# Optimization experiments

Hardware: AMD Instinct MI355X
Metric: run time of the kernel (lower is better)

Reference implementation:

```python
import jax, jax.numpy as jnp
import numpy as np

NEG_SLOPE = 0.2  # PyG GATConv default negative_slope


def _glorot(key, shape):
    fan = shape[0]
    return jax.random.normal(key, shape, dtype=jnp.float32) / np.sqrt(fan)


def setup_inputs() -> dict:
    key = jax.random.key(0)
    ks = jax.random.split(key, 32)
    N, E, C_IN, C_H, C_OUT = 20000, 320000, 128, 640, 2
    inp = {
        "x": jax.random.normal(ks[0], (N, C_IN), dtype=jnp.float32),
        "edge_index": jax.random.randint(ks[1], (2, E), 0, N, dtype=jnp.int64),
    }
    dims = [(C_IN, C_H), (C_H, C_H), (C_H, C_H), (C_H, C_H), (C_H, C_OUT)]
    for i, (ci, co) in enumerate(dims, start=1):
        k = jax.random.split(ks[1 + i], 4)
        inp[f"W{i}"] = _glorot(k[0], (ci, co))
        inp[f"as{i}"] = _glorot(k[1], (co,))
        inp[f"ad{i}"] = _glorot(k[2], (co,))
        inp[f"b{i}"] = jnp.zeros((co,), dtype=jnp.float32)
    return inp


def _gat_conv(h, W, a_src, a_dst, b, src, dst, N):
    # h: [N, Ci] -> hW: [N, Co]
    hW = h @ W
    # per-edge attention logit: LeakyReLU(alpha_src[j] + alpha_dst[i]) for edge j->i
    e = jax.nn.leaky_relu((hW @ a_src)[src] + (hW @ a_dst)[dst], NEG_SLOPE)
    # segment softmax over incoming edges of each dst node (self-loops guarantee nonempty)
    m = jax.ops.segment_max(e, dst, num_segments=N)
    ex = jnp.exp(e - m[dst])
    den = jax.ops.segment_sum(ex, dst, num_segments=N)
    alpha = ex / den[dst]
    # weighted scatter-add of source messages
    out = jax.ops.segment_sum(alpha[:, None] * hW[src], dst, num_segments=N)
    return out + b


def reference(x, edge_index, W1, as1, ad1, b1, W2, as2, ad2, b2, W3, as3, ad3, b3,
              W4, as4, ad4, b4, W5, as5, ad5, b5):
    N = x.shape[0]
    # PyG GATConv default add_self_loops=True
    loops = jnp.arange(N, dtype=edge_index.dtype)
    ei = jnp.concatenate([edge_index, jnp.stack([loops, loops])], axis=1)
    src, dst = ei[0], ei[1]
    h = jax.nn.relu(_gat_conv(x, W1, as1, ad1, b1, src, dst, N))
    h = jax.nn.relu(_gat_conv(h, W2, as2, ad2, b2, src, dst, N))
    h = jax.nn.relu(_gat_conv(h, W3, as3, ad3, b3, src, dst, N))
    h = jax.nn.relu(_gat_conv(h, W4, as4, ad4, b4, src, dst, N))
    # dropout in eval mode = identity
    return _gat_conv(h, W5, as5, ad5, b5, src, dst, N)
```

## Files before the change

### kernel.cpp

```cpp
#include <hip/hip_runtime.h>
#include <math.h>

#define N_NODES 20000
#define MPAD 20096
#define E_EDGES 320000
#define ET (E_EDGES + N_NODES)
#define C_HID 640
#define C_IN 128
#define NEG_SLOPE 0.2f

#define NXB 157
#define NYB 10
#define NXB_FULL 152
#define IDS_MAIN 1520

typedef __attribute__((ext_vector_type(8))) short bf16x8;
typedef __attribute__((ext_vector_type(4))) float f32x4;

__device__ __forceinline__ float leaky(float x) { return x > 0.f ? x : NEG_SLOPE * x; }

__device__ __forceinline__ unsigned short f2bf(float f) {
    unsigned u = __float_as_uint(f);
    unsigned r = (u + 0x7fffu + ((u >> 16) & 1u)) >> 16;
    return (unsigned short)r;
}
__device__ __forceinline__ float bf2f(unsigned short h) {
    return __uint_as_float(((unsigned)h) << 16);
}

__device__ __forceinline__ void gld16(const void* g, void* l) {
    __builtin_amdgcn_global_load_lds((const __attribute__((address_space(1))) unsigned int*)g,
                                     (__attribute__((address_space(3))) unsigned int*)l,
                                     16, 0, 0);
}

__device__ __forceinline__ void decode_xy(int id, int& bx, int& by) {
    if (id < IDS_MAIN) {
        int g = id / 80;
        bx = g * 8 + (id & 7);
        by = (id % 80) >> 3;
    } else {
        int v = id - IDS_MAIN;
        bx = NXB_FULL + v % 5;
        by = v / 5;
    }
}

__global__ void k_zero(int* p, int n) {
    int i = blockIdx.x * blockDim.x + threadIdx.x;
    if (i < n) p[i] = 0;
}

__global__ void k_count(const int* __restrict__ ei, int* __restrict__ counts) {
    int j = blockIdx.x * blockDim.x + threadIdx.x;
    if (j >= ET) return;
    int d = (j < E_EDGES) ? ei[E_EDGES + j] : (j - E_EDGES);
    atomicAdd(&counts[d], 1);
}

__global__ __launch_bounds__(1024) void k_scan(int* __restrict__ counts,
                                               int* __restrict__ rowptr) {
    __shared__ int part[1024];
    int t = threadIdx.x;
    int base = t * 20;
    int incl[20];
    int s = 0;
#pragma unroll
    for (int k = 0; k < 20; k++) {
        int i = base + k;
        int v = (i < N_NODES) ? counts[i] : 0;
        s += v;
        incl[k] = s;
    }
    part[t] = s;
    __syncthreads();
    for (int off = 1; off < 1024; off <<= 1) {
        int x = (t >= off) ? part[t - off] : 0;
        __syncthreads();
        part[t] += x;
        __syncthreads();
    }
    int prefix = (t == 0) ? 0 : part[t - 1];
    if (t == 0) rowptr[0] = 0;
#pragma unroll
    for (int k = 0; k < 20; k++) {
        int i = base + k;
        if (i < N_NODES) {
            rowptr[i + 1] = prefix + incl[k];
            counts[i] = (k == 0) ? prefix : prefix + incl[k - 1];
        }
    }
}

__global__ void k_fill(const int* __restrict__ ei, int* __restrict__ cursor, int* __restrict__ col) {
    int j = blockIdx.x * blockDim.x + threadIdx.x;
    if (j >= ET) return;
    int s, d;
    if (j < E_EDGES) { s = ei[j]; d = ei[E_EDGES + j]; }
    else { s = d = j - E_EDGES; }
    int pos = atomicAdd(&cursor[d], 1);
    col[pos] = s;
}

__global__ __launch_bounds__(256) void k_splitWT(const float* __restrict__ W,
                                                 unsigned short* __restrict__ Wth,
                                                 unsigned short* __restrict__ Wtl, int K,
                                                 float* __restrict__ zbuf, int zn) {
    if (zbuf) {
        int tid = ((blockIdx.y * gridDim.x + blockIdx.x) * 256 + threadIdx.x) * 2;
        if (tid < zn) zbuf[tid] = 0.f;
        if (tid + 1 < zn) zbuf[tid + 1] = 0.f;
    }
    __shared__ float tile[64][65];
    int t = threadIdx.x;
    int ki = blockIdx.x * 64, ni = blockIdx.y * 64;
    int tr = t >> 2;
    int tc = (t & 3) * 16;
#pragma unroll
    for (int q = 0; q < 4; ++q) {
        float4 v = *(const float4*)&W[(size_t)(ki + tr) * C_HID + ni + tc + q * 4];
        tile[tr][tc + q * 4 + 0] = v.x;
        tile[tr][tc + q * 4 + 1] = v.y;
        tile[tr][tc + q * 4 + 2] = v.z;
        tile[tr][tc + q * 4 + 3] = v.w;
    }
    __syncthreads();
    unsigned short hh[16], ll[16];
#pragma unroll
    for (int j = 0; j < 16; ++j) {
        float w = tile[tc + j][tr];
        unsigned short h = f2bf(w);
        hh[j] = h;
        ll[j] = f2bf(w - bf2f(h));
    }
    size_t o = (size_t)(ni + tr) * K + ki + tc;
#pragma unroll
    for (int q = 0; q < 4; ++q) {
        *(ushort4*)&Wth[o + q * 4] = make_ushort4(hh[q*4], hh[q*4+1], hh[q*4+2], hh[q*4+3]);
        *(ushort4*)&Wtl[o + q * 4] = make_ushort4(ll[q*4], ll[q*4+1], ll[q*4+2], ll[q*4+3]);
    }
}

__global__ void k_padzero(unsigned short* __restrict__ xah, unsigned short* __restrict__ xal,
                          unsigned short* __restrict__ ph, unsigned short* __restrict__ pl) {
    int idx = blockIdx.x * blockDim.x + threadIdx.x;
    const int nx = (MPAD - N_NODES) * C_IN;
    const int np = (MPAD - N_NODES) * C_HID;
    if (idx < nx) {
        xah[N_NODES * C_IN + idx] = 0;
        xal[N_NODES * C_IN + idx] = 0;
    }
    if (idx < np) {
        ph[N_NODES * C_HID + idx] = 0;
        pl[N_NODES * C_HID + idx] = 0;
    }
}

__global__ void k_wa(const float* __restrict__ W, const float* __restrict__ a_s,
                     const float* __restrict__ a_d,
                     float* __restrict__ ws_, float* __restrict__ wd_) {
    int wave = (blockIdx.x * blockDim.x + threadIdx.x) >> 6;
    int lane = threadIdx.x & 63;
    if (wave >= C_IN) return;
    const float* row = W + (size_t)wave * C_HID;
    float s = 0.f, d = 0.f;
#pragma unroll
    for (int c = lane; c < C_HID; c += 64) {
        float w = row[c];
        s = fmaf(w, a_s[c], s);
        d = fmaf(w, a_d[c], d);
    }
    for (int o = 32; o; o >>= 1) { s += __shfl_xor(s, o); d += __shfl_xor(d, o); }
    if (lane == 0) { ws_[wave] = s; wd_[wave] = d; }
}

__global__ __launch_bounds__(256) void k_logitx(const float* __restrict__ x,
                                                const float* __restrict__ ws_,
                                                const float* __restrict__ wd_,
                                                float* __restrict__ as_, float* __restrict__ ad_) {
    int wave = (blockIdx.x * blockDim.x + threadIdx.x) >> 6;
    int lane = threadIdx.x & 63;
    if (wave >= N_NODES) return;
    float2 xv = ((const float2*)(x + (size_t)wave * C_IN))[lane];
    float2 wsv = ((const float2*)ws_)[lane];
    float2 wdv = ((const float2*)wd_)[lane];
    float s = xv.x * wsv.x + xv.y * wsv.y;
    float d = xv.x * wdv.x + xv.y * wdv.y;
    for (int o = 32; o; o >>= 1) { s += __shfl_xor(s, o); d += __shfl_xor(d, o); }
    if (lane == 0) { as_[wave] = s; ad_[wave] = d; }
}

__global__ __launch_bounds__(256) void k_alpha(const float* __restrict__ as_,
                                               const float* __restrict__ ad_,
                                               const int* __restrict__ rowptr,
                                               const int* __restrict__ col,
                                               float* __restrict__ alpha) {
    int wave = (blockIdx.x * blockDim.x + threadIdx.x) >> 6;
    int lane = threadIdx.x & 63;
    if (wave >= N_NODES) return;
    int start = rowptr[wave], end = rowptr[wave + 1];
    float adi = ad_[wave];
    float m = -1e30f;
    for (int j = start + lane; j < end; j += 64)
        m = fmaxf(m, leaky(as_[col[j]] + adi));
    for (int o = 32; o; o >>= 1) m = fmaxf(m, __shfl_xor(m, o));
    float den = 0.f;
    for (int j = start + lane; j < end; j += 64)
        den += __expf(leaky(as_[col[j]] + adi) - m);
    for (int o = 32; o; o >>= 1) den += __shfl_xor(den, o);
    float inv = 1.f / den;
    for (int j = start + lane; j < end; j += 64)
        alpha[j] = __expf(leaky(as_[col[j]] + adi) - m) * inv;
}

__global__ __launch_bounds__(256) void k_mfma_gemm(
    const unsigned short* __restrict__ Ahi, const unsigned short* __restrict__ Alo,
    const unsigned short* __restrict__ Bth, const unsigned short* __restrict__ Btl,
    float* __restrict__ C, int K, int M,
    const float* __restrict__ asrc, const float* __restrict__ adst,
    float* __restrict__ as_, float* __restrict__ ad_) {
    __shared__ unsigned short lds[12288];
    const int t = threadIdx.x;
    const int lane = t & 63, wv = t >> 6;
    const int wm = wv >> 1, wn = wv & 1;
    const int quad = lane >> 4, cl = lane & 15;
    int bx, by;
    decode_xy(blockIdx.x, bx, by);
    const int rowBase = bx * 128;
    const int colBase = by * 64;
    const int r4 = t >> 2;
    const int cswz = ((t & 3) ^ ((r4 >> 1) & 3)) * 8;
    const int rshift = (cl >> 1) & 3;

    f32x4 acc[4][2];
#pragma unroll
    for (int i = 0; i < 4; i++)
#pragma unroll
        for (int j = 0; j < 2; j++)
            acc[i][j] = (f32x4){0.f, 0.f, 0.f, 0.f};

    for (int k0 = 0; k0 < K; k0 += 32) {
        __syncthreads();
#pragma unroll
        for (int p = 0; p < 2; ++p) {
            int row = p * 64 + r4;
            size_t ga = (size_t)(rowBase + row) * K + k0 + cswz;
            int lo = row * 32 + (t & 3) * 8;
            gld16(Ahi + ga, &lds[lo]);
            gld16(Alo + ga, &lds[4096 + lo]);
        }
        {
            size_t gb = (size_t)(colBase + r4) * K + k0 + cswz;
            int lo = r4 * 32 + (t & 3) * 8;
            gld16(Bth + gb, &lds[8192 + lo]);
            gld16(Btl + gb, &lds[10240 + lo]);
        }
        __syncthreads();

        bf16x8 ah[4], al[4], bh[2], bl[2];
#pragma unroll
        for (int i = 0; i < 4; ++i) {
            int am = (wm * 64 + i * 16 + cl) * 32 + (quad ^ rshift) * 8;
            ah[i] = *(const bf16x8*)&lds[am];
            al[i] = *(const bf16x8*)&lds[4096 + am];
        }
#pragma unroll
        for (int j = 0; j < 2; ++j) {
            int bn = (wn * 32 + j * 16 + cl) * 32 + (quad ^ rshift) * 8;
            bh[j] = *(const bf16x8*)&lds[8192 + bn];
            bl[j] = *(const bf16x8*)&lds[10240 + bn];
        }
#pragma unroll
        for (int i = 0; i < 4; ++i)
#pragma unroll
            for (int j = 0; j < 2; ++j) {
                acc[i][j] = __builtin_amdgcn_mfma_f32_16x16x32_bf16(ah[i], bh[j], acc[i][j], 0, 0, 0);
                acc[i][j] = __builtin_amdgcn_mfma_f32_16x16x32_bf16(ah[i], bl[j], acc[i][j], 0, 0, 0);
                acc[i][j] = __builtin_amdgcn_mfma_f32_16x16x32_bf16(al[i], bh[j], acc[i][j], 0, 0, 0);
            }
    }

#pragma unroll
    for (int i = 0; i < 4; ++i)
#pragma unroll
        for (int j = 0; j < 2; ++j) {
            int colC = colBase + wn * 32 + j * 16 + cl;
#pragma unroll
            for (int rr = 0; rr < 4; ++rr) {
                int rowC = rowBase + wm * 64 + i * 16 + quad * 4 + rr;
                if (rowC < M) C[(size_t)rowC * C_HID + colC] = acc[i][j][rr];
            }
        }

    float av[2], dv[2];
#pragma unroll
    for (int j = 0; j < 2; ++j) {
        int cn = colBase + wn * 32 + j * 16 + cl;
        av[j] = asrc[cn];
        dv[j] = adst[cn];
    }
#pragma unroll
    for (int i = 0; i < 4; ++i)
#pragma unroll
        for (int rr = 0; rr < 4; ++rr) {
            float s = 0.f, d = 0.f;
#pragma unroll
            for (int j = 0; j < 2; ++j) {
                float v = acc[i][j][rr];
                s = fmaf(v, av[j], s);
                d = fmaf(v, dv[j], d);
            }
#pragma unroll
            for (int o = 8; o >= 1; o >>= 1) {
                s += __shfl_xor(s, o);
                d += __shfl_xor(d, o);
            }
            int rowC = rowBase + wm * 64 + i * 16 + quad * 4 + rr;
            if (cl == 0 && rowC < M) {
                atomicAdd(&as_[rowC], s);
                atomicAdd(&ad_[rowC], d);
            }
        }
}

__global__ __launch_bounds__(256) void k_mfma_gemm_pair(
    const unsigned short* __restrict__ Ahi, const unsigned short* __restrict__ Alo,
    const unsigned short* __restrict__ Bth, const unsigned short* __restrict__ Btl,
    unsigned short* __restrict__ Oh, unsigned short* __restrict__ Ol,
    const float* __restrict__ bias, int K, int M) {
    __shared__ unsigned short lds[12288];
    const int t = threadIdx.x;
    const int lane = t & 63, wv = t >> 6;
    const int wm = wv >> 1, wn = wv & 1;
    const int quad = lane >> 4, cl = lane & 15;
    int bx, by;
    decode_xy(blockIdx.x, bx, by);
    const int rowBase = bx * 128;
    const int colBase = by * 64;
    const int r4 = t >> 2;
    const int cswz = ((t & 3) ^ ((r4 >> 1) & 3)) * 8;
    const int rshift = (cl >> 1) & 3;

    f32x4 acc[4][2];
#pragma unroll
    for (int i = 0; i < 4; i++)
#pragma unroll
        for (int j = 0; j < 2; j++)
            acc[i][j] = (f32x4){0.f, 0.f, 0.f, 0.f};

    for (int k0 = 0; k0 < K; k0 += 32) {
        __syncthreads();
#pragma unroll
        for (int p = 0; p < 2; ++p) {
            int row = p * 64 + r4;
            size_t ga = (size_t)(rowBase + row) * K + k0 + cswz;
            int lo = row * 32 + (t & 3) * 8;
            gld16(Ahi + ga, &lds[lo]);
            gld16(Alo + ga, &lds[4096 + lo]);
        }
        {
            size_t gb = (size_t)(colBase + r4) * K + k0 + cswz;
            int lo = r4 * 32 + (t & 3) * 8;
            gld16(Bth + gb, &lds[8192 + lo]);
            gld16(Btl + gb, &lds[10240 + lo]);
        }
        __syncthreads();

        bf16x8 ah[4], al[4], bh[2], bl[2];
#pragma unroll
        for (int i = 0; i < 4; ++i) {
            int am = (wm * 64 + i * 16 + cl) * 32 + (quad ^ rshift) * 8;
            ah[i] = *(const bf16x8*)&lds[am];
            al[i] = *(const bf16x8*)&lds[4096 + am];
        }
#pragma unroll
        for (int j = 0; j < 2; ++j) {
            int bn = (wn * 32 + j * 16 + cl) * 32 + (quad ^ rshift) * 8;
            bh[j] = *(const bf16x8*)&lds[8192 + bn];
            bl[j] = *(const bf16x8*)&lds[10240 + bn];
        }
#pragma unroll
        for (int i = 0; i < 4; ++i)
#pragma unroll
            for (int j = 0; j < 2; ++j) {
                acc[i][j] = __builtin_amdgcn_mfma_f32_16x16x32_bf16(ah[i], bh[j], acc[i][j], 0, 0, 0);
                acc[i][j] = __builtin_amdgcn_mfma_f32_16x16x32_bf16(ah[i], bl[j], acc[i][j], 0, 0, 0);
                acc[i][j] = __builtin_amdgcn_mfma_f32_16x16x32_bf16(al[i], bh[j], acc[i][j], 0, 0, 0);
            }
    }

#pragma unroll
    for (int j = 0; j < 2; ++j) {
        int colC = colBase + wn * 32 + j * 16 + cl;
        float bv = bias[colC];
#pragma unroll
        for (int i = 0; i < 4; ++i)
#pragma unroll
            for (int rr = 0; rr < 4; ++rr) {
                int rowC = rowBase + wm * 64 + i * 16 + quad * 4 + rr;
                if (rowC < M) {
                    float v = fmaxf(acc[i][j][rr] + bv, 0.f);
                    unsigned short h = f2bf(v);
                    Oh[(size_t)rowC * C_HID + colC] = h;
                    Ol[(size_t)rowC * C_HID + colC] = f2bf(v - bf2f(h));
                }
            }
    }
}

__global__ __launch_bounds__(256) void k_gather64(const float* __restrict__ hW,
                                                  const float* __restrict__ alpha,
                                                  const int* __restrict__ rowptr,
                                                  const int* __restrict__ col,
                                                  const float* __restrict__ bias,
                                                  unsigned short* __restrict__ outh,
                                                  unsigned short* __restrict__ outl) {
    int lane = threadIdx.x & 63;
    int node = __builtin_amdgcn_readfirstlane(blockIdx.x * 4 + (threadIdx.x >> 6));
    int c = blockIdx.y;
    if (node >= N_NODES) return;
    int start = rowptr[node], end = rowptr[node + 1];
    const float* base = hW + c * 64 + lane;
    float ax = 0.f;

    int j0 = start;
    for (; j0 + 16 <= end; j0 += 16) {
        int cv[16];
        float av[16];
#pragma unroll
        for (int q = 0; q < 16; ++q) { cv[q] = col[j0 + q]; av[q] = alpha[j0 + q]; }
        float r[16];
#pragma unroll
        for (int q = 0; q < 16; ++q) r[q] = base[(size_t)cv[q] * C_HID];
#pragma unroll
        for (int q = 0; q < 16; ++q) ax = fmaf(av[q], r[q], ax);
    }
    if (j0 < end) {
        int jb = end - 16; if (jb < 0) jb = 0;
        int cv[16];
        float av[16];
#pragma unroll
        for (int q = 0; q < 16; ++q) {
            cv[q] = col[jb + q];
            av[q] = (jb + q >= j0) ? alpha[jb + q] : 0.f;
        }
        float r[16];
#pragma unroll
        for (int q = 0; q < 16; ++q) r[q] = base[(size_t)cv[q] * C_HID];
#pragma unroll
        for (int q = 0; q < 16; ++q) ax = fmaf(av[q], r[q], ax);
    }

    float v0 = fmaxf(ax + bias[c * 64 + lane], 0.f);
    unsigned short h0 = f2bf(v0);
    size_t o = (size_t)node * C_HID + c * 64 + lane;
    outh[o] = h0;
    outl[o] = f2bf(v0 - bf2f(h0));
}

__global__ __launch_bounds__(256) void k_gather_x(const float* __restrict__ x,
                                                  const float* __restrict__ alpha,
                                                  const int* __restrict__ rowptr,
                                                  const int* __restrict__ col,
                                                  unsigned short* __restrict__ outh,
                                                  unsigned short* __restrict__ outl) {
    int lane = threadIdx.x & 63;
    int node = __builtin_amdgcn_readfirstlane(blockIdx.x * 4 + (threadIdx.x >> 6));
    if (node >= N_NODES) return;
    int start = rowptr[node], end = rowptr[node + 1];
    const float* base = x + lane * 2;
    float ax = 0.f, ay = 0.f;

    int j0 = start;
    for (; j0 + 8 <= end; j0 += 8) {
        int cv[8];
        float av[8];
#pragma unroll
        for (int q = 0; q < 8; ++q) { cv[q] = col[j0 + q]; av[q] = alpha[j0 + q]; }
        float2 r[8];
#pragma unroll
        for (int q = 0; q < 8; ++q) r[q] = *(const float2*)(base + (size_t)cv[q] * C_IN);
#pragma unroll
        for (int q = 0; q < 8; ++q) {
            ax = fmaf(av[q], r[q].x, ax);
            ay = fmaf(av[q], r[q].y, ay);
        }
    }
    if (j0 < end) {
        int jb = end - 8; if (jb < 0) jb = 0;
        int cv[8];
        float av[8];
#pragma unroll
        for (int q = 0; q < 8; ++q) {
            cv[q] = col[jb + q];
            av[q] = (jb + q >= j0) ? alpha[jb + q] : 0.f;
        }
        float2 r[8];
#pragma unroll
        for (int q = 0; q < 8; ++q) r[q] = *(const float2*)(base + (size_t)cv[q] * C_IN);
#pragma unroll
        for (int q = 0; q < 8; ++q) {
            ax = fmaf(av[q], r[q].x, ax);
            ay = fmaf(av[q], r[q].y, ay);
        }
    }

    unsigned short h0 = f2bf(ax), h1 = f2bf(ay);
    size_t o = (size_t)node * C_IN + lane * 2;
    *(ushort2*)&outh[o] = make_ushort2(h0, h1);
    *(ushort2*)&outl[o] = make_ushort2(f2bf(ax - bf2f(h0)), f2bf(ay - bf2f(h1)));
}

__global__ __launch_bounds__(256) void k_gemm2(const unsigned short* __restrict__ hh,
                                               const unsigned short* __restrict__ hl,
                                               const float* __restrict__ W,
                                               const float* __restrict__ asrc,
                                               const float* __restrict__ adst,
                                               float* __restrict__ hW5,
                                               float* __restrict__ as_,
                                               float* __restrict__ ad_) {
    int wave = (blockIdx.x * blockDim.x + threadIdx.x) >> 6;
    int lane = threadIdx.x & 63;
    if (wave >= N_NODES) return;
    const ushort2* rh = (const ushort2*)(hh + (size_t)wave * C_HID);
    const ushort2* rl = (const ushort2*)(hl + (size_t)wave * C_HID);
    float a0 = 0.f, a1 = 0.f;
#pragma unroll
    for (int k2 = lane; k2 < C_HID / 2; k2 += 64) {
        ushort2 h2 = rh[k2];
        ushort2 l2 = rl[k2];
        float v0 = bf2f(h2.x) + bf2f(l2.x);
        float v1 = bf2f(h2.y) + bf2f(l2.y);
        int k = k2 * 2;
        a0 = fmaf(v0, W[k * 2 + 0], a0);
        a1 = fmaf(v0, W[k * 2 + 1], a1);
        a0 = fmaf(v1, W[k * 2 + 2], a0);
        a1 = fmaf(v1, W[k * 2 + 3], a1);
    }
    for (int o = 32; o; o >>= 1) { a0 += __shfl_xor(a0, o); a1 += __shfl_xor(a1, o); }
    if (lane == 0) {
        hW5[wave * 2 + 0] = a0;
        hW5[wave * 2 + 1] = a1;
        as_[wave] = a0 * asrc[0] + a1 * asrc[1];
        ad_[wave] = a0 * adst[0] + a1 * adst[1];
    }
}

__global__ __launch_bounds__(256) void k_agg2(const float* __restrict__ hW5,
                                              const float* __restrict__ as_,
                                              const float* __restrict__ ad_,
                                              const int* __restrict__ rowptr,
                                              const int* __restrict__ col,
                                              const float* __restrict__ bias,
                                              float* __restrict__ out) {
    int wv = threadIdx.x >> 6, lane = threadIdx.x & 63;
    int node = blockIdx.x * 4 + wv;
    if (node >= N_NODES) return;
    int start = rowptr[node], end = rowptr[node + 1];
    int deg = end - start;
    float adi = ad_[node];
    float o0, o1;
    if (deg <= 64) {
        int cv = col[start + min(lane, deg - 1)];
        float logit = (lane < deg) ? leaky(as_[cv] + adi) : -1e30f;
        float m = logit;
#pragma unroll
        for (int o = 32; o; o >>= 1) m = fmaxf(m, __shfl_xor(m, o));
        float ex = __expf(logit - m);
        float den = ex;
#pragma unroll
        for (int o = 32; o; o >>= 1) den += __shfl_xor(den, o);
        float al = ex / den;
        float2 hv = make_float2(0.f, 0.f);
        if (lane < deg) hv = *(const float2*)&hW5[cv * 2];
        o0 = al * hv.x; o1 = al * hv.y;
#pragma unroll
        for (int o = 32; o; o >>= 1) { o0 += __shfl_xor(o0, o); o1 += __shfl_xor(o1, o); }
    } else {
        float m = -1e30f;
        for (int j = start + lane; j < end; j += 64)
            m = fmaxf(m, leaky(as_[col[j]] + adi));
        for (int o = 32; o; o >>= 1) m = fmaxf(m, __shfl_xor(m, o));
        float den = 0.f;
        for (int j = start + lane; j < end; j += 64)
            den += __expf(leaky(as_[col[j]] + adi) - m);
        for (int o = 32; o; o >>= 1) den += __shfl_xor(den, o);
        float inv = 1.f / den;
        o0 = 0.f; o1 = 0.f;
        for (int j = start + lane; j < end; j += 64) {
            int s = col[j];
            float al = __expf(leaky(as_[s] + adi) - m) * inv;
            o0 = fmaf(al, hW5[s * 2 + 0], o0);
            o1 = fmaf(al, hW5[s * 2 + 1], o1);
        }
        for (int o = 32; o; o >>= 1) { o0 += __shfl_xor(o0, o); o1 += __shfl_xor(o1, o); }
    }
    if (lane == 0) {
        out[node * 2 + 0] = o0 + bias[0];
        out[node * 2 + 1] = o1 + bias[1];
    }
}

extern "C" void kernel_launch(void* const* d_in, const int* in_sizes, int n_in,
                              void* d_out, int out_size, void* d_ws, size_t ws_size,
                              hipStream_t stream) {
    const float* x   = (const float*)d_in[0];
    const int*   ei  = (const int*)d_in[1];
    const float* W[5]  = {(const float*)d_in[2],  (const float*)d_in[6],
                          (const float*)d_in[10], (const float*)d_in[14],
                          (const float*)d_in[18]};
    const float* As[5] = {(const float*)d_in[3],  (const float*)d_in[7],
                          (const float*)d_in[11], (const float*)d_in[15],
                          (const float*)d_in[19]};
    const float* Ad[5] = {(const float*)d_in[4],  (const float*)d_in[8],
                          (const float*)d_in[12], (const float*)d_in[16],
                          (const float*)d_in[20]};
    const float* Bi[5] = {(const float*)d_in[5],  (const float*)d_in[9],
                          (const float*)d_in[13], (const float*)d_in[17],
                          (const float*)d_in[21]};
    float* out = (float*)d_out;

    char* w = (char*)d_ws;
    float* bufX = (float*)w;                 w += (size_t)N_NODES * C_HID * 4;
    unsigned short* xa_hi = (unsigned short*)bufX;
    unsigned short* xa_lo = xa_hi + (size_t)MPAD * C_IN;
    unsigned short* pair_hi = (unsigned short*)w; w += (size_t)MPAD * C_HID * 2;
    unsigned short* pair_lo = (unsigned short*)w; w += (size_t)MPAD * C_HID * 2;
    unsigned short* Wth = (unsigned short*)w;     w += (size_t)C_HID * C_HID * 2;
    unsigned short* Wtl = (unsigned short*)w;     w += (size_t)C_HID * C_HID * 2;
    float* as_  = (float*)w;  w += N_NODES * 4;
    float* ad_  = (float*)w;  w += N_NODES * 4;
    float* hW5  = (float*)w;  w += N_NODES * 2 * 4;
    float* ws_  = (float*)w;  w += C_IN * 4;
    float* wd_  = (float*)w;  w += C_IN * 4;
    float* alpha = (float*)w; w += ET * 4;
    int* rowptr = (int*)w;    w += (N_NODES + 1) * 4 + 12;
    int* counts = (int*)w;    w += N_NODES * 4;
    int* col    = (int*)w;    w += ET * 4;

    const int TB = 256;
    k_zero<<<(N_NODES + TB - 1) / TB, TB, 0, stream>>>(counts, N_NODES);
    k_count<<<(ET + TB - 1) / TB, TB, 0, stream>>>(ei, counts);
    k_scan<<<1, 1024, 0, stream>>>(counts, rowptr);
    k_fill<<<(ET + TB - 1) / TB, TB, 0, stream>>>(ei, counts, col);

    k_padzero<<<((MPAD - N_NODES) * C_HID + TB - 1) / TB, TB, 0, stream>>>(xa_hi, xa_lo, pair_hi, pair_lo);

    const int gemmBlocks = NXB * NYB;
    dim3 gathGrid(N_NODES / 4, 10);
    int nodeWaveBlocks = (N_NODES + 3) / 4;

    k_splitWT<<<dim3(C_IN / 64, C_HID / 64), TB, 0, stream>>>(W[0], Wth, Wtl, C_IN, (float*)0, 0);
    k_wa<<<32, TB, 0, stream>>>(W[0], As[0], Ad[0], ws_, wd_);
    k_logitx<<<nodeWaveBlocks, TB, 0, stream>>>(x, ws_, wd_, as_, ad_);
    k_alpha<<<nodeWaveBlocks, TB, 0, stream>>>(as_, ad_, rowptr, col, alpha);
    k_gather_x<<<nodeWaveBlocks, TB, 0, stream>>>(x, alpha, rowptr, col, xa_hi, xa_lo);
    k_mfma_gemm_pair<<<gemmBlocks, TB, 0, stream>>>(xa_hi, xa_lo, Wth, Wtl,
                                                    pair_hi, pair_lo, Bi[0], C_IN, N_NODES);

    for (int l = 1; l <= 3; ++l) {
        k_splitWT<<<dim3(C_HID / 64, C_HID / 64), TB, 0, stream>>>(W[l], Wth, Wtl, C_HID,
                                                                   as_, 2 * N_NODES);
        k_mfma_gemm<<<gemmBlocks, TB, 0, stream>>>(pair_hi, pair_lo, Wth, Wtl, bufX, C_HID, N_NODES,
                                                   As[l], Ad[l], as_, ad_);
        k_alpha<<<nodeWaveBlocks, TB, 0, stream>>>(as_, ad_, rowptr, col, alpha);
        k_gather64<<<gathGrid, TB, 0, stream>>>(bufX, alpha, rowptr, col, Bi[l], pair_hi, pair_lo);
    }

    k_gemm2<<<nodeWaveBlocks, TB, 0, stream>>>(pair_hi, pair_lo, W[4], As[4], Ad[4], hW5, as_, ad_);
    k_agg2<<<nodeWaveBlocks, TB, 0, stream>>>(hW5, as_, ad_, rowptr, col, Bi[4], out);
}
```

Before: 763.0 us.

## Double GEMM K-tile to 64 with XOR swizzle and fuse layer-1 softmax into gather

```diff
diff --git a/kernel.cpp b/kernel.cpp
--- a/kernel.cpp
+++ b/kernel.cpp
@@ -219,7 +219,7 @@
     float* __restrict__ C, int K, int M,
     const float* __restrict__ asrc, const float* __restrict__ adst,
     float* __restrict__ as_, float* __restrict__ ad_) {
-    __shared__ unsigned short lds[12288];
+    __shared__ unsigned short lds[24576];
     const int t = threadIdx.x;
     const int lane = t & 63, wv = t >> 6;
     const int wm = wv >> 1, wn = wv & 1;
@@ -228,9 +228,8 @@
     decode_xy(blockIdx.x, bx, by);
     const int rowBase = bx * 128;
     const int colBase = by * 64;
-    const int r4 = t >> 2;
-    const int cswz = ((t & 3) ^ ((r4 >> 1) & 3)) * 8;
-    const int rshift = (cl >> 1) & 3;
+    const int sr = t >> 3;
+    const int scg = ((t & 7) ^ (sr & 7)) * 8;
 
     f32x4 acc[4][2];
 #pragma unroll
@@ -239,45 +238,52 @@
         for (int j = 0; j < 2; j++)
             acc[i][j] = (f32x4){0.f, 0.f, 0.f, 0.f};
 
-    for (int k0 = 0; k0 < K; k0 += 32) {
+    for (int k0 = 0; k0 < K; k0 += 64) {
         __syncthreads();
 #pragma unroll
+        for (int p = 0; p < 4; ++p) {
+            int r = p * 32 + sr;
+            size_t ga = (size_t)(rowBase + r) * K + k0 + scg;
+            int lo = p * 2048 + t * 8;
+            gld16(Ahi + ga, &lds[lo]);
+            gld16(Alo + ga, &lds[8192 + lo]);
+        }
+#pragma unroll
         for (int p = 0; p < 2; ++p) {
-            int row = p * 64 + r4;
-            size_t ga = (size_t)(rowBase + row) * K + k0 + cswz;
-            int lo = row * 32 + (t & 3) * 8;
-            gld16(Ahi + ga, &lds[lo]);
-            gld16(Alo + ga, &lds[4096 + lo]);
-        }
-        {
-            size_t gb = (size_t)(colBase + r4) * K + k0 + cswz;
-            int lo = r4 * 32 + (t & 3) * 8;
-            gld16(Bth + gb, &lds[8192 + lo]);
-            gld16(Btl + gb, &lds[10240 + lo]);
+            int r = p * 32 + sr;
+            size_t gb = (size_t)(colBase + r) * K + k0 + scg;
+            int lo = p * 2048 + t * 8;
+            gld16(Bth + gb, &lds[16384 + lo]);
+            gld16(Btl + gb, &lds[20480 + lo]);
         }
         __syncthreads();
 
-        bf16x8 ah[4], al[4], bh[2], bl[2];
-#pragma unroll
-        for (int i = 0; i < 4; ++i) {
-            int am = (wm * 64 + i * 16 + cl) * 32 + (quad ^ rshift) * 8;
-            ah[i] = *(const bf16x8*)&lds[am];
-            al[i] = *(const bf16x8*)&lds[4096 + am];
-        }
-#pragma unroll
-        for (int j = 0; j < 2; ++j) {
-            int bn = (wn * 32 + j * 16 + cl) * 32 + (quad ^ rshift) * 8;
-            bh[j] = *(const bf16x8*)&lds[8192 + bn];
-            bl[j] = *(const bf16x8*)&lds[10240 + bn];
-        }
-#pragma unroll
-        for (int i = 0; i < 4; ++i)
+#pragma unroll
+        for (int ks = 0; ks < 2; ++ks) {
+            bf16x8 ah[4], al[4], bh[2], bl[2];
+#pragma unroll
+            for (int i = 0; i < 4; ++i) {
+                int row = wm * 64 + i * 16 + cl;
+                int am = row * 64 + (((ks * 4 + quad) ^ (row & 7)) * 8);
+                ah[i] = *(const bf16x8*)&lds[am];
+                al[i] = *(const bf16x8*)&lds[8192 + am];
+            }
 #pragma unroll
             for (int j = 0; j < 2; ++j) {
-                acc[i][j] = __builtin_amdgcn_mfma_f32_16x16x32_bf16(ah[i], bh[j], acc[i][j], 0, 0, 0);
-                acc[i][j] = __builtin_amdgcn_mfma_f32_16x16x32_bf16(ah[i], bl[j], acc[i][j], 0, 0, 0);
-                acc[i][j] = __builtin_amdgcn_mfma_f32_16x16x32_bf16(al[i], bh[j], acc[i][j], 0, 0, 0);
-            }
+                int row = wn * 32 + j * 16 + cl;
+                int bn = row * 64 + (((ks * 4 + quad) ^ (row & 7)) * 8);
+                bh[j] = *(const bf16x8*)&lds[16384 + bn];
+                bl[j] = *(const bf16x8*)&lds[20480 + bn];
+            }
+#pragma unroll
+            for (int i = 0; i < 4; ++i)
+#pragma unroll
+                for (int j = 0; j < 2; ++j) {
+                    acc[i][j] = __builtin_amdgcn_mfma_f32_16x16x32_bf16(ah[i], bh[j], acc[i][j], 0, 0, 0);
+                    acc[i][j] = __builtin_amdgcn_mfma_f32_16x16x32_bf16(ah[i], bl[j], acc[i][j], 0, 0, 0);
+                    acc[i][j] = __builtin_amdgcn_mfma_f32_16x16x32_bf16(al[i], bh[j], acc[i][j], 0, 0, 0);
+                }
+        }
     }
 
 #pragma unroll
@@ -328,7 +334,7 @@
     const unsigned short* __restrict__ Bth, const unsigned short* __restrict__ Btl,
     unsigned short* __restrict__ Oh, unsigned short* __restrict__ Ol,
     const float* __restrict__ bias, int K, int M) {
-    __shared__ unsigned short lds[12288];
+    __shared__ unsigned short lds[24576];
     const int t = threadIdx.x;
     const int lane = t & 63, wv = t >> 6;
     const int wm = wv >> 1, wn = wv & 1;
@@ -337,9 +343,8 @@
     decode_xy(blockIdx.x, bx, by);
     const int rowBase = bx * 128;
     const int colBase = by * 64;
-    const int r4 = t >> 2;
-    const int cswz = ((t & 3) ^ ((r4 >> 1) & 3)) * 8;
-    const int rshift = (cl >> 1) & 3;
+    const int sr = t >> 3;
+    const int scg = ((t & 7) ^ (sr & 7)) * 8;
 
     f32x4 acc[4][2];
 #pragma unroll
@@ -348,45 +353,52 @@
         for (int j = 0; j < 2; j++)
             acc[i][j] = (f32x4){0.f, 0.f, 0.f, 0.f};
 
-    for (int k0 = 0; k0 < K; k0 += 32) {
+    for (int k0 = 0; k0 < K; k0 += 64) {
         __syncthreads();
 #pragma unroll
+        for (int p = 0; p < 4; ++p) {
+            int r = p * 32 + sr;
+            size_t ga = (size_t)(rowBase + r) * K + k0 + scg;
+            int lo = p * 2048 + t * 8;
+            gld16(Ahi + ga, &lds[lo]);
+            gld16(Alo + ga, &lds[8192 + lo]);
+        }
+#pragma unroll
         for (int p = 0; p < 2; ++p) {
-            int row = p * 64 + r4;
-            size_t ga = (size_t)(rowBase + row) * K + k0 + cswz;
-            int lo = row * 32 + (t & 3) * 8;
-            gld16(Ahi + ga, &lds[lo]);
-            gld16(Alo + ga, &lds[4096 + lo]);
-        }
-        {
-            size_t gb = (size_t)(colBase + r4) * K + k0 + cswz;
-            int lo = r4 * 32 + (t & 3) * 8;
-            gld16(Bth + gb, &lds[8192 + lo]);
-            gld16(Btl + gb, &lds[10240 + lo]);
+            int r = p * 32 + sr;
+            size_t gb = (size_t)(colBase + r) * K + k0 + scg;
+            int lo = p * 2048 + t * 8;
+            gld16(Bth + gb, &lds[16384 + lo]);
+            gld16(Btl + gb, &lds[20480 + lo]);
         }
         __syncthreads();
 
-        bf16x8 ah[4], al[4], bh[2], bl[2];
-#pragma unroll
-        for (int i = 0; i < 4; ++i) {
-            int am = (wm * 64 + i * 16 + cl) * 32 + (quad ^ rshift) * 8;
-            ah[i] = *(const bf16x8*)&lds[am];
-            al[i] = *(const bf16x8*)&lds[4096 + am];
-        }
-#pragma unroll
-        for (int j = 0; j < 2; ++j) {
-            int bn = (wn * 32 + j * 16 + cl) * 32 + (quad ^ rshift) * 8;
-            bh[j] = *(const bf16x8*)&lds[8192 + bn];
-            bl[j] = *(const bf16x8*)&lds[10240 + bn];
-        }
-#pragma unroll
-        for (int i = 0; i < 4; ++i)
+#pragma unroll
+        for (int ks = 0; ks < 2; ++ks) {
+            bf16x8 ah[4], al[4], bh[2], bl[2];
+#pragma unroll
+            for (int i = 0; i < 4; ++i) {
+                int row = wm * 64 + i * 16 + cl;
+                int am = row * 64 + (((ks * 4 + quad) ^ (row & 7)) * 8);
+                ah[i] = *(const bf16x8*)&lds[am];
+                al[i] = *(const bf16x8*)&lds[8192 + am];
+            }
 #pragma unroll
             for (int j = 0; j < 2; ++j) {
-                acc[i][j] = __builtin_amdgcn_mfma_f32_16x16x32_bf16(ah[i], bh[j], acc[i][j], 0, 0, 0);
-                acc[i][j] = __builtin_amdgcn_mfma_f32_16x16x32_bf16(ah[i], bl[j], acc[i][j], 0, 0, 0);
-                acc[i][j] = __builtin_amdgcn_mfma_f32_16x16x32_bf16(al[i], bh[j], acc[i][j], 0, 0, 0);
-            }
+                int row = wn * 32 + j * 16 + cl;
+                int bn = row * 64 + (((ks * 4 + quad) ^ (row & 7)) * 8);
+                bh[j] = *(const bf16x8*)&lds[16384 + bn];
+                bl[j] = *(const bf16x8*)&lds[20480 + bn];
+            }
+#pragma unroll
+            for (int i = 0; i < 4; ++i)
+#pragma unroll
+                for (int j = 0; j < 2; ++j) {
+                    acc[i][j] = __builtin_amdgcn_mfma_f32_16x16x32_bf16(ah[i], bh[j], acc[i][j], 0, 0, 0);
+                    acc[i][j] = __builtin_amdgcn_mfma_f32_16x16x32_bf16(ah[i], bl[j], acc[i][j], 0, 0, 0);
+                    acc[i][j] = __builtin_amdgcn_mfma_f32_16x16x32_bf16(al[i], bh[j], acc[i][j], 0, 0, 0);
+                }
+        }
     }
 
 #pragma unroll
@@ -459,49 +471,68 @@
 }
 
 __global__ __launch_bounds__(256) void k_gather_x(const float* __restrict__ x,
-                                                  const float* __restrict__ alpha,
+                                                  const float* __restrict__ as_,
+                                                  const float* __restrict__ ad_,
                                                   const int* __restrict__ rowptr,
                                                   const int* __restrict__ col,
                                                   unsigned short* __restrict__ outh,
                                                   unsigned short* __restrict__ outl) {
-    int lane = threadIdx.x & 63;
-    int node = __builtin_amdgcn_readfirstlane(blockIdx.x * 4 + (threadIdx.x >> 6));
+    int wv = threadIdx.x >> 6, lane = threadIdx.x & 63;
+    int node = blockIdx.x * 4 + wv;
     if (node >= N_NODES) return;
     int start = rowptr[node], end = rowptr[node + 1];
+    int deg = end - start;
     const float* base = x + lane * 2;
     float ax = 0.f, ay = 0.f;
-
-    int j0 = start;
-    for (; j0 + 8 <= end; j0 += 8) {
-        int cv[8];
-        float av[8];
-#pragma unroll
-        for (int q = 0; q < 8; ++q) { cv[q] = col[j0 + q]; av[q] = alpha[j0 + q]; }
-        float2 r[8];
-#pragma unroll
-        for (int q = 0; q < 8; ++q) r[q] = *(const float2*)(base + (size_t)cv[q] * C_IN);
-#pragma unroll
-        for (int q = 0; q < 8; ++q) {
-            ax = fmaf(av[q], r[q].x, ax);
-            ay = fmaf(av[q], r[q].y, ay);
-        }
-    }
-    if (j0 < end) {
-        int jb = end - 8; if (jb < 0) jb = 0;
-        int cv[8];
-        float av[8];
-#pragma unroll
-        for (int q = 0; q < 8; ++q) {
-            cv[q] = col[jb + q];
-            av[q] = (jb + q >= j0) ? alpha[jb + q] : 0.f;
-        }
-        float2 r[8];
-#pragma unroll
-        for (int q = 0; q < 8; ++q) r[q] = *(const float2*)(base + (size_t)cv[q] * C_IN);
-#pragma unroll
-        for (int q = 0; q < 8; ++q) {
-            ax = fmaf(av[q], r[q].x, ax);
-            ay = fmaf(av[q], r[q].y, ay);
+    float adi = ad_[node];
+
+    if (deg <= 64) {
+        int col_v = col[start + min(lane, deg - 1)];
+        float asv = as_[col_v];
+        float logit = (lane < deg) ? leaky(asv + adi) : -1e30f;
+        float m = logit;
+#pragma unroll
+        for (int o = 32; o; o >>= 1) m = fmaxf(m, __shfl_xor(m, o));
+        float ex = __expf(logit - m);
+        float den = ex;
+#pragma unroll
+        for (int o = 32; o; o >>= 1) den += __shfl_xor(den, o);
+        float alpha_v = ex / den;
+
+        for (int e0 = 0; e0 < deg; e0 += 8) {
+            float2 r[8];
+            float a[8];
+#pragma unroll
+            for (int q = 0; q < 8; ++q) {
+                int e = e0 + q;
+                int ec = min(e, deg - 1);
+                int s = __shfl(col_v, ec);
+                float ar = __shfl(alpha_v, ec);
+                a[q] = (e < deg) ? ar : 0.f;
+                r[q] = *(const float2*)(base + (size_t)s * C_IN);
+            }
+#pragma unroll
+            for (int q = 0; q < 8; ++q) {
+                ax = fmaf(a[q], r[q].x, ax);
+                ay = fmaf(a[q], r[q].y, ay);
+            }
+        }
+    } else {
+        float m = -1e30f;
+        for (int j = start + lane; j < end; j += 64)
+            m = fmaxf(m, leaky(as_[col[j]] + adi));
+        for (int o = 32; o; o >>= 1) m = fmaxf(m, __shfl_xor(m, o));
+        float den = 0.f;
+        for (int j = start + lane; j < end; j += 64)
+            den += __expf(leaky(as_[col[j]] + adi) - m);
+        for (int o = 32; o; o >>= 1) den += __shfl_xor(den, o);
+        float inv = 1.f / den;
+        for (int j = start; j < end; ++j) {
+            int s = col[j];
+            float a = __expf(leaky(as_[s] + adi) - m) * inv;
+            float2 r = *(const float2*)(base + (size_t)s * C_IN);
+            ax = fmaf(a, r.x, ax);
+            ay = fmaf(a, r.y, ay);
         }
     }
 
@@ -653,8 +684,7 @@
     k_splitWT<<<dim3(C_IN / 64, C_HID / 64), TB, 0, stream>>>(W[0], Wth, Wtl, C_IN, (float*)0, 0);
     k_wa<<<32, TB, 0, stream>>>(W[0], As[0], Ad[0], ws_, wd_);
     k_logitx<<<nodeWaveBlocks, TB, 0, stream>>>(x, ws_, wd_, as_, ad_);
-    k_alpha<<<nodeWaveBlocks, TB, 0, stream>>>(as_, ad_, rowptr, col, alpha);
-    k_gather_x<<<nodeWaveBlocks, TB, 0, stream>>>(x, alpha, rowptr, col, xa_hi, xa_lo);
+    k_gather_x<<<nodeWaveBlocks, TB, 0, stream>>>(x, as_, ad_, rowptr, col, xa_hi, xa_lo);
     k_mfma_gemm_pair<<<gemmBlocks, TB, 0, stream>>>(xa_hi, xa_lo, Wth, Wtl,
                                                     pair_hi, pair_lo, Bi[0], C_IN, N_NODES);
 
```

New measurement: 715.1 us (median of 2 runs). 1.07x faster.
